# Kernel optimization log

Hardware: AMD Instinct MI355X
Metric: run time of the kernel (lower is better)

## Reference

```python
import jax, jax.numpy as jnp
import numpy as np

D = 256; NH = 8; NL = 4; NP = 4; DFF = 1024; BS = 8; NQ = 300
DH = D // NH
EPS = 1e-5
SPATIAL = np.array([[100, 150], [50, 75], [25, 38], [13, 19]], dtype=np.int64)  # (H, W) per level
SIZES = (SPATIAL[:, 0] * SPATIAL[:, 1])
S = int(SIZES.sum())  # 19947
LSI = np.concatenate([[0], np.cumsum(SIZES)[:-1]]).astype(np.int64)


def setup_inputs() -> dict:
    key = jax.random.key(0)
    ks = iter(jax.random.split(key, 48))
    def nrm(shape, s=0.02):
        return jax.random.normal(next(ks), shape, jnp.float32) * s
    return {
        "tgt": jax.random.normal(next(ks), (BS, NQ, D), jnp.float32),
        "tgt_query_pos": jax.random.normal(next(ks), (BS, NQ, D), jnp.float32),
        "tgt_reference_points": jax.random.uniform(next(ks), (BS, NQ, NL, 2), jnp.float32),
        "memory": jax.random.normal(next(ks), (BS, S, D), jnp.float32),
        "memory_key_padding_mask": jnp.zeros((BS, S), jnp.bool_),
        "memory_spatial_shapes": jnp.asarray(SPATIAL),
        "memory_level_start_index": jnp.asarray(LSI),
        # self-attention (nn.MultiheadAttention) params
        "in_proj_w": nrm((3 * D, D)), "in_proj_b": jnp.zeros((3 * D,), jnp.float32),
        "out_proj_w": nrm((D, D)), "out_proj_b": jnp.zeros((D,), jnp.float32),
        # layernorms
        "norm1_g": jnp.ones((D,), jnp.float32), "norm1_b": jnp.zeros((D,), jnp.float32),
        "norm2_g": jnp.ones((D,), jnp.float32), "norm2_b": jnp.zeros((D,), jnp.float32),
        "norm3_g": jnp.ones((D,), jnp.float32), "norm3_b": jnp.zeros((D,), jnp.float32),
        # MSDeformAttn params
        "samp_off_w": nrm((NH * NL * NP * 2, D)), "samp_off_b": nrm((NH * NL * NP * 2,), 0.5),
        "attn_wt_w": nrm((NH * NL * NP, D)), "attn_wt_b": jnp.zeros((NH * NL * NP,), jnp.float32),
        "value_w": nrm((D, D)), "value_b": jnp.zeros((D,), jnp.float32),
        "outp_w": nrm((D, D)), "outp_b": jnp.zeros((D,), jnp.float32),
        # FFN params
        "lin1_w": nrm((DFF, D)), "lin1_b": jnp.zeros((DFF,), jnp.float32),
        "lin2_w": nrm((D, DFF)), "lin2_b": jnp.zeros((D,), jnp.float32),
    }


def _ln(x, g, b):
    m = x.mean(-1, keepdims=True)
    v = ((x - m) ** 2).mean(-1, keepdims=True)
    return (x - m) / jnp.sqrt(v + EPS) * g + b


def _self_attn(tgt, pos, in_w, in_b, ow, ob):
    bs, nq, _ = tgt.shape
    qk = tgt + pos
    qw, kw, vw = jnp.split(in_w, 3, axis=0)
    qb, kb, vb = jnp.split(in_b, 3)
    proj = lambda x, w, b: (x @ w.T + b).reshape(bs, nq, NH, DH)
    qh, kh, vh = proj(qk, qw, qb), proj(qk, kw, kb), proj(tgt, vw, vb)
    logits = jnp.einsum('bqhd,bkhd->bhqk', qh, kh) / np.sqrt(DH).astype(np.float32)
    a = jax.nn.softmax(logits, axis=-1)
    o = jnp.einsum('bhqk,bkhd->bqhd', a, vh).reshape(bs, nq, D)
    return o @ ow.T + ob


def _msdeform(query, ref, memory, pad_mask, so_w, so_b, aw_w, aw_b, vw, vb, ow, ob):
    bs, nq, _ = query.shape
    value = memory @ vw.T + vb
    value = jnp.where(pad_mask[..., None], 0.0, value).reshape(bs, S, NH, DH)
    off = (query @ so_w.T + so_b).reshape(bs, nq, NH, NL, NP, 2)
    aw = jax.nn.softmax((query @ aw_w.T + aw_b).reshape(bs, nq, NH, NL * NP), axis=-1)
    aw = aw.reshape(bs, nq, NH, NL, NP)
    # offset normalizer is (W, H) per level
    normalizer = jnp.asarray(SPATIAL[:, ::-1].copy(), jnp.float32)
    locs = ref[:, :, None, :, None, :] + off / normalizer[None, None, None, :, None, :]
    out = jnp.zeros((bs, nq, NH, DH), jnp.float32)
    for l in range(NL):
        Hl, Wl = int(SPATIAL[l, 0]), int(SPATIAL[l, 1])
        s0 = int(LSI[l])
        v = value[:, s0:s0 + Hl * Wl]  # [bs, Hl*Wl, NH, DH]
        # grid_sample(align_corners=False) pixel mapping
        x = locs[:, :, :, l, :, 0] * Wl - 0.5  # [bs, nq, NH, NP]
        y = locs[:, :, :, l, :, 1] * Hl - 0.5
        x0f, y0f = jnp.floor(x), jnp.floor(y)
        tx, ty = x - x0f, y - y0f
        x0, y0 = x0f.astype(jnp.int32), y0f.astype(jnp.int32)
        samp = jnp.zeros(x.shape + (DH,), jnp.float32)
        for dy, dx, w in ((0, 0, (1 - ty) * (1 - tx)), (0, 1, (1 - ty) * tx),
                          (1, 0, ty * (1 - tx)), (1, 1, ty * tx)):
            xi, yi = x0 + dx, y0 + dy
            valid = (xi >= 0) & (xi < Wl) & (yi >= 0) & (yi < Hl)  # zero padding
            idx = jnp.clip(yi, 0, Hl - 1) * Wl + jnp.clip(xi, 0, Wl - 1)
            idx2 = idx.swapaxes(2, 3).reshape(bs, nq * NP, NH)
            g = jnp.take_along_axis(v, idx2[..., None], axis=1)  # [bs, nq*NP, NH, DH]
            g = g.reshape(bs, nq, NP, NH, DH).transpose(0, 1, 3, 2, 4)
            samp = samp + g * (w * valid)[..., None]
        out = out + jnp.einsum('bqhp,bqhpd->bqhd', aw[:, :, :, l], samp)
    return out.reshape(bs, nq, D) @ ow.T + ob


def reference(tgt, tgt_query_pos, tgt_reference_points, memory, memory_key_padding_mask,
              memory_spatial_shapes, memory_level_start_index,
              in_proj_w, in_proj_b, out_proj_w, out_proj_b,
              norm1_g, norm1_b, norm2_g, norm2_b, norm3_g, norm3_b,
              samp_off_w, samp_off_b, attn_wt_w, attn_wt_b,
              value_w, value_b, outp_w, outp_b,
              lin1_w, lin1_b, lin2_w, lin2_b):
    # self-cross ordering (self_cross=True), eval mode (dropout=identity)
    t2 = _self_attn(tgt, tgt_query_pos, in_proj_w, in_proj_b, out_proj_w, out_proj_b)
    tgt = _ln(tgt + t2, norm2_g, norm2_b)
    t2 = _msdeform(tgt + tgt_query_pos, tgt_reference_points, memory, memory_key_padding_mask,
                   samp_off_w, samp_off_b, attn_wt_w, attn_wt_b, value_w, value_b, outp_w, outp_b)
    tgt = _ln(tgt + t2, norm1_g, norm1_b)
    t2 = jax.nn.relu(tgt @ lin1_w.T + lin1_b) @ lin2_w.T + lin2_b
    return _ln(tgt + t2, norm3_g, norm3_b)
```

## Files before the change

### kernel.cpp

```cpp
#include <hip/hip_runtime.h>
#include <hip/hip_bf16.h>

#define D_   256
#define NH_  8
#define NL_  4
#define NP_  4
#define DFF_ 1024
#define BS_  8
#define NQ_  300
#define DH_  32
#define S_TOT 19947
#define EPS_ 1e-5f

typedef __bf16 bf16x8 __attribute__((ext_vector_type(8)));
typedef __bf16 bf16x4 __attribute__((ext_vector_type(4)));
typedef float  f32x4  __attribute__((ext_vector_type(4)));

#define W_INW  0
#define W_OUTW 196608
#define W_SOW  262144
#define W_AWW  327680
#define W_VW   360448
#define W_OPW  425984
#define W_L1W  491520
#define W_L2W  753664
#define W_TOT  1015808

__global__ __launch_bounds__(256) void cast_w_kernel(
    const float* __restrict__ s_inw, const float* __restrict__ s_outw,
    const float* __restrict__ s_sow, const float* __restrict__ s_aww,
    const float* __restrict__ s_vw,  const float* __restrict__ s_opw,
    const float* __restrict__ s_l1w, const float* __restrict__ s_l2w,
    __bf16* __restrict__ dst)
{
    const int i = (blockIdx.x * 256 + threadIdx.x) * 4;
    if (i >= W_TOT) return;
    const float* s; int off;
    if      (i < W_OUTW) { s = s_inw;  off = W_INW;  }
    else if (i < W_SOW)  { s = s_outw; off = W_OUTW; }
    else if (i < W_AWW)  { s = s_sow;  off = W_SOW;  }
    else if (i < W_VW)   { s = s_aww;  off = W_AWW;  }
    else if (i < W_OPW)  { s = s_vw;   off = W_VW;   }
    else if (i < W_L1W)  { s = s_opw;  off = W_OPW;  }
    else if (i < W_L2W)  { s = s_l1w;  off = W_L1W;  }
    else                 { s = s_l2w;  off = W_L2W;  }
    const float4 v = *(const float4*)(s + (i - off));
    bf16x4 o;
    o[0] = (__bf16)v.x; o[1] = (__bf16)v.y;
    o[2] = (__bf16)v.z; o[3] = (__bf16)v.w;
    *(bf16x4*)(dst + i) = o;
}

__global__ __launch_bounds__(256) void rearrange_vw_kernel(
    const __bf16* __restrict__ W, __bf16* __restrict__ Wf)
{
    const int g = blockIdx.x * 256 + threadIdx.x;
    const int l = g & 63;
    const int t = (g >> 6) & 15;
    const int s = g >> 10;
    const int row = t * 16 + (l & 15);
    const int col = s * 32 + (l >> 4) * 8;
    *(bf16x8*)(Wf + (size_t)g * 8) = *(const bf16x8*)(W + (size_t)row * 256 + col);
}

__global__ __launch_bounds__(512, 4) void gemm_value(
    const float* __restrict__ A, const __bf16* __restrict__ Wf,
    const float* __restrict__ bias, __hip_bfloat16* __restrict__ C, int M)
{
    __shared__ __align__(16) __bf16 As[2][16][264];
    const int tid = threadIdx.x;
    const int wave = tid >> 6, lane = tid & 63;
    const int frow = lane & 15;
    const int k8 = (lane >> 4) * 8;

    bf16x8 bB[2][8];
#pragma unroll
    for (int j = 0; j < 2; ++j) {
        const int t = wave * 2 + j;
#pragma unroll
        for (int s = 0; s < 8; ++s)
            bB[j][s] = *(const bf16x8*)(Wf + ((size_t)(s * 16 + t) * 64 + lane) * 8);
    }
    float bb0 = bias[wave * 32 + frow];
    float bb1 = bias[wave * 32 + 16 + frow];

    const int nt = (M + 15) >> 4;
    const int stride = gridDim.x;
    int tile = blockIdx.x;

    const int srow = tid >> 5;
    const int scol = (tid & 31) * 8;

    {
        int gr = tile * 16 + srow; if (gr >= M) gr = M - 1;
        const float* ap = A + (size_t)gr * 256 + scol;
        const float4 a0 = *(const float4*)ap;
        const float4 a1 = *(const float4*)(ap + 4);
        bf16x8 o;
        o[0] = (__bf16)a0.x; o[1] = (__bf16)a0.y;
        o[2] = (__bf16)a0.z; o[3] = (__bf16)a0.w;
        o[4] = (__bf16)a1.x; o[5] = (__bf16)a1.y;
        o[6] = (__bf16)a1.z; o[7] = (__bf16)a1.w;
        *(bf16x8*)&As[0][srow][scol] = o;
    }
    __syncthreads();

    int buf = 0;
    for (; tile < nt; tile += stride, buf ^= 1) {
        const int nxt = tile + stride;
        const bool have_nxt = nxt < nt;
        float4 p0, p1;
        if (have_nxt) {
            int gr = nxt * 16 + srow; if (gr >= M) gr = M - 1;
            const float* ap = A + (size_t)gr * 256 + scol;
            p0 = *(const float4*)ap;
            p1 = *(const float4*)(ap + 4);
        }

        f32x4 acc0 = (f32x4){0.f, 0.f, 0.f, 0.f};
        f32x4 acc1 = acc0;
#pragma unroll
        for (int s = 0; s < 8; ++s) {
            const bf16x8 aF = *(const bf16x8*)&As[buf][frow][s * 32 + k8];
            acc0 = __builtin_amdgcn_mfma_f32_16x16x32_bf16(aF, bB[0][s], acc0, 0, 0, 0);
            acc1 = __builtin_amdgcn_mfma_f32_16x16x32_bf16(aF, bB[1][s], acc1, 0, 0, 0);
        }

        const int m0 = tile * 16;
        const int row0 = (lane >> 4) * 4;
        const int col0 = wave * 32 + frow;
#pragma unroll
        for (int r = 0; r < 4; ++r) {
            const int gr = m0 + row0 + r;
            if (gr < M) {
                __hip_bfloat16* cp = C + (size_t)gr * 256 + col0;
                cp[0]  = __float2bfloat16(acc0[r] + bb0);
                cp[16] = __float2bfloat16(acc1[r] + bb1);
            }
        }

        if (have_nxt) {
            bf16x8 o;
            o[0] = (__bf16)p0.x; o[1] = (__bf16)p0.y;
            o[2] = (__bf16)p0.z; o[3] = (__bf16)p0.w;
            o[4] = (__bf16)p1.x; o[5] = (__bf16)p1.y;
            o[6] = (__bf16)p1.z; o[7] = (__bf16)p1.w;
            *(bf16x8*)&As[buf ^ 1][srow][scol] = o;
        }
        __syncthreads();
    }
}

__global__ __launch_bounds__(256) void gemm_small(
    const float* __restrict__ A, const float* __restrict__ A2,
    const __bf16* __restrict__ W, const float* __restrict__ bias,
    float* __restrict__ C, int M, int N, int K, int relu,
    const float* __restrict__ bias2, float* __restrict__ C2, int N1)
{
    __shared__ __align__(16) __bf16 As[64][40];
    __shared__ __align__(16) __bf16 Bs[64][40];
    const int tid = threadIdx.x;
    const int wave = tid >> 6, lane = tid & 63;
    const int m0 = blockIdx.x * 64, n0 = blockIdx.y * 64;
    const int frow = lane & 15, fk = (lane >> 4) * 8;

    f32x4 acc[4];
#pragma unroll
    for (int j = 0; j < 4; ++j) acc[j] = (f32x4){0.f, 0.f, 0.f, 0.f};

    const int ar = tid >> 2;
    const int ak = (tid & 3) * 8;
    const bool a_ok = (m0 + ar) < M;

    for (int k0 = 0; k0 < K; k0 += 32) {
        float4 a0 = make_float4(0,0,0,0), a1 = a0;
        if (a_ok) {
            const float* ap = A + (size_t)(m0 + ar) * K + k0 + ak;
            a0 = *(const float4*)ap;
            a1 = *(const float4*)(ap + 4);
            if (A2) {
                const float* ap2 = A2 + (size_t)(m0 + ar) * K + k0 + ak;
                const float4 c0 = *(const float4*)ap2;
                const float4 c1 = *(const float4*)(ap2 + 4);
                a0.x += c0.x; a0.y += c0.y; a0.z += c0.z; a0.w += c0.w;
                a1.x += c1.x; a1.y += c1.y; a1.z += c1.z; a1.w += c1.w;
            }
        }
        const bf16x8 b8 = *(const bf16x8*)(W + (size_t)(n0 + ar) * K + k0 + ak);

        __syncthreads();
        bf16x8 w0;
        w0[0] = (__bf16)a0.x; w0[1] = (__bf16)a0.y; w0[2] = (__bf16)a0.z; w0[3] = (__bf16)a0.w;
        w0[4] = (__bf16)a1.x; w0[5] = (__bf16)a1.y; w0[6] = (__bf16)a1.z; w0[7] = (__bf16)a1.w;
        *(bf16x8*)&As[ar][ak] = w0;
        *(bf16x8*)&Bs[ar][ak] = b8;
        __syncthreads();

        const bf16x8 aF = *(const bf16x8*)&As[wave * 16 + frow][fk];
#pragma unroll
        for (int j = 0; j < 4; ++j) {
            const bf16x8 bF = *(const bf16x8*)&Bs[j * 16 + frow][fk];
            acc[j] = __builtin_amdgcn_mfma_f32_16x16x32_bf16(aF, bF, acc[j], 0, 0, 0);
        }
    }

    const int row = m0 + wave * 16 + (lane >> 4) * 4;
#pragma unroll
    for (int j = 0; j < 4; ++j) {
        const int col = n0 + j * 16 + frow;
        float* dst; const float* bsrc; int strideC, ccol;
        if (!C2 || col < N1) { dst = C;  bsrc = bias;  strideC = N1;     ccol = col; }
        else                 { dst = C2; bsrc = bias2; strideC = N - N1; ccol = col - N1; }
        const float bb = bsrc[ccol];
#pragma unroll
        for (int r = 0; r < 4; ++r) {
            if (row + r >= M) continue;
            float val = acc[j][r] + bb;
            if (relu) val = fmaxf(val, 0.f);
            dst[(size_t)(row + r) * strideC + ccol] = val;
        }
    }
}

__global__ __launch_bounds__(256) void attn_fused_kernel(
    const float* __restrict__ qk, const float* __restrict__ v,
    float* __restrict__ attn)
{
    __shared__ __align__(16) __bf16 Vt[32][328];
    __shared__ __align__(16) __bf16 Ps[64][328];
    const int qt = blockIdx.x, bh = blockIdx.y;
    const int b = bh >> 3, h = bh & 7;
    const int tid = threadIdx.x;
    const int wave = tid >> 6, lane = tid & 63;
    const float scale = 0.17677669529663687f;

    {
        const int d = tid & 31;
        for (int kk = tid >> 5; kk < NQ_; kk += 8)
            Vt[d][kk] = (__bf16)v[(size_t)(b * NQ_ + kk) * 256 + h * 32 + d];
        for (int i = tid; i < 32 * 20; i += 256)
            Vt[i & 31][300 + (i >> 5)] = (__bf16)0.f;
        for (int i = tid; i < 64 * 16; i += 256)
            Ps[i & 63][304 + (i >> 6)] = (__bf16)0.f;
    }

    const int m = qt * 64 + wave * 16 + (lane & 15);
    const int k8 = (lane >> 4) * 8;

    bf16x8 aF = {};
    if (m < NQ_) {
        const float* qp = qk + (size_t)(b * NQ_ + m) * 512 + h * 32 + k8;
        const float4 q0 = *(const float4*)qp;
        const float4 q1 = *(const float4*)(qp + 4);
        aF[0] = (__bf16)q0.x; aF[1] = (__bf16)q0.y;
        aF[2] = (__bf16)q0.z; aF[3] = (__bf16)q0.w;
        aF[4] = (__bf16)q1.x; aF[5] = (__bf16)q1.y;
        aF[6] = (__bf16)q1.z; aF[7] = (__bf16)q1.w;
    }

    f32x4 c[19];
#pragma unroll
    for (int t = 0; t < 19; ++t) {
        const int n = t * 16 + (lane & 15);
        bf16x8 bF = {};
        if (n < NQ_) {
            const float* kp = qk + (size_t)(b * NQ_ + n) * 512 + 256 + h * 32 + k8;
            const float4 k0 = *(const float4*)kp;
            const float4 k1 = *(const float4*)(kp + 4);
            bF[0] = (__bf16)k0.x; bF[1] = (__bf16)k0.y;
            bF[2] = (__bf16)k0.z; bF[3] = (__bf16)k0.w;
            bF[4] = (__bf16)k1.x; bF[5] = (__bf16)k1.y;
            bF[6] = (__bf16)k1.z; bF[7] = (__bf16)k1.w;
        }
        f32x4 z = (f32x4){0.f, 0.f, 0.f, 0.f};
        c[t] = __builtin_amdgcn_mfma_f32_16x16x32_bf16(aF, bF, z, 0, 0, 0);
    }

    const int myc = lane & 15;
#pragma unroll
    for (int t = 0; t < 19; ++t) {
        const bool ok = (t * 16 + myc) < NQ_;
#pragma unroll
        for (int r = 0; r < 4; ++r)
            c[t][r] = ok ? c[t][r] * scale : -1e30f;
    }

    float mx[4] = {-1e30f, -1e30f, -1e30f, -1e30f};
#pragma unroll
    for (int t = 0; t < 19; ++t)
#pragma unroll
        for (int r = 0; r < 4; ++r) mx[r] = fmaxf(mx[r], c[t][r]);
#pragma unroll
    for (int off = 8; off; off >>= 1)
#pragma unroll
        for (int r = 0; r < 4; ++r)
            mx[r] = fmaxf(mx[r], __shfl_xor(mx[r], off, 64));

    float sum[4] = {0.f, 0.f, 0.f, 0.f};
#pragma unroll
    for (int t = 0; t < 19; ++t)
#pragma unroll
        for (int r = 0; r < 4; ++r) {
            const float e = __expf(c[t][r] - mx[r]);
            c[t][r] = e;
            sum[r] += e;
        }
#pragma unroll
    for (int off = 8; off; off >>= 1)
#pragma unroll
        for (int r = 0; r < 4; ++r)
            sum[r] += __shfl_xor(sum[r], off, 64);
    float inv[4];
#pragma unroll
    for (int r = 0; r < 4; ++r) inv[r] = 1.f / sum[r];

    const int lrow0 = wave * 16 + (lane >> 4) * 4;
#pragma unroll
    for (int t = 0; t < 19; ++t) {
        const int col = t * 16 + myc;
#pragma unroll
        for (int r = 0; r < 4; ++r)
            Ps[lrow0 + r][col] = (__bf16)(c[t][r] * inv[r]);
    }
    __syncthreads();

    const int lm = wave * 16 + (lane & 15);
    f32x4 acc0 = (f32x4){0.f, 0.f, 0.f, 0.f};
    f32x4 acc1 = acc0;
#pragma unroll
    for (int k0 = 0; k0 < 320; k0 += 32) {
        const bf16x8 pF = *(const bf16x8*)&Ps[lm][k0 + k8];
        const bf16x8 b0 = *(const bf16x8*)&Vt[lane & 15][k0 + k8];
        const bf16x8 b1 = *(const bf16x8*)&Vt[16 + (lane & 15)][k0 + k8];
        acc0 = __builtin_amdgcn_mfma_f32_16x16x32_bf16(pF, b0, acc0, 0, 0, 0);
        acc1 = __builtin_amdgcn_mfma_f32_16x16x32_bf16(pF, b1, acc1, 0, 0, 0);
    }

    const int row0 = qt * 64 + lrow0;
    const int col = lane & 15;
#pragma unroll
    for (int r = 0; r < 4; ++r) {
        if (row0 + r >= NQ_) continue;
        float* op = attn + (size_t)(b * NQ_ + row0 + r) * 256 + h * 32;
        op[col]      = acc0[r];
        op[col + 16] = acc1[r];
    }
}

__global__ __launch_bounds__(256) void ln_kernel(
    const float* __restrict__ x, const float* __restrict__ res,
    const float* __restrict__ g, const float* __restrict__ bt,
    float* __restrict__ out,
    const float* __restrict__ pos, float* __restrict__ out2)
{
    const int row = blockIdx.x;
    const int tid = threadIdx.x;
    const size_t idx = (size_t)row * D_ + tid;
    float v = x[idx] + (res ? res[idx] : 0.f);

    __shared__ float red[4];
    float s = v;
#pragma unroll
    for (int off = 32; off; off >>= 1) s += __shfl_xor(s, off, 64);
    if ((tid & 63) == 0) red[tid >> 6] = s;
    __syncthreads();
    const float mean = (red[0] + red[1] + red[2] + red[3]) * (1.f / D_);
    const float c = v - mean;
    __syncthreads();

    float s2 = c * c;
#pragma unroll
    for (int off = 32; off; off >>= 1) s2 += __shfl_xor(s2, off, 64);
    if ((tid & 63) == 0) red[tid >> 6] = s2;
    __syncthreads();
    const float var = (red[0] + red[1] + red[2] + red[3]) * (1.f / D_);

    const float y = c * rsqrtf(var + EPS_) * g[tid] + bt[tid];
    out[idx] = y;
    if (out2) out2[idx] = y + pos[idx];
}

__global__ __launch_bounds__(256) void msdeform_kernel(
    const float* __restrict__ offs, const float* __restrict__ awl,
    const float* __restrict__ refp, const __hip_bfloat16* __restrict__ value,
    float* __restrict__ samp)
{
    const int half = threadIdx.x >> 7;
    const int row = blockIdx.x * 2 + half;
    const int b = row / NQ_;
    const int t = threadIdx.x & 127;
    const int h = t >> 4, d2 = t & 15;

    __shared__ float off_s[2][256];
    __shared__ float aw_s[2][128];
    __shared__ float ref_s[2][8];
    off_s[half][t]       = offs[(size_t)row * 256 + t];
    off_s[half][t + 128] = offs[(size_t)row * 256 + t + 128];
    aw_s[half][t]        = awl[(size_t)row * 128 + t];
    if (t < 8) ref_s[half][t] = refp[(size_t)row * 8 + t];
    __syncthreads();

    float mx = -1e30f;
#pragma unroll
    for (int i = 0; i < 16; ++i) mx = fmaxf(mx, aw_s[half][h * 16 + i]);
    float sum = 0.f;
#pragma unroll
    for (int i = 0; i < 16; ++i) sum += __expf(aw_s[half][h * 16 + i] - mx);
    const float winv = 1.f / sum;

    const int Hs[4] = {100, 50, 25, 13};
    const int Wl_[4] = {150, 75, 38, 19};
    const int S0[4] = {0, 15000, 18750, 19700};

    float o0 = 0.f, o1 = 0.f;
    const __hip_bfloat16* vbase = value + ((size_t)b * S_TOT) * D_ + h * 32 + d2 * 2;

#pragma unroll
    for (int l = 0; l < NL_; ++l) {
        const int Hl = Hs[l], Wl = Wl_[l];
        const float rx = ref_s[half][l * 2], ry = ref_s[half][l * 2 + 1];
        const __hip_bfloat16* vl = vbase + (size_t)S0[l] * D_;
#pragma unroll
        for (int p = 0; p < NP_; ++p) {
            const int oi = ((h * NL_ + l) * NP_ + p) * 2;
            const float lx = rx + off_s[half][oi] / (float)Wl;
            const float ly = ry + off_s[half][oi + 1] / (float)Hl;
            const float x = lx * Wl - 0.5f;
            const float y = ly * Hl - 0.5f;
            const float x0f = floorf(x), y0f = floorf(y);
            const float tx = x - x0f, ty = y - y0f;
            const int x0 = (int)x0f, y0 = (int)y0f;
            const float aw = __expf(aw_s[half][h * 16 + l * 4 + p] - mx) * winv;

            float s0 = 0.f, s1 = 0.f;
#pragma unroll
            for (int cc = 0; cc < 4; ++cc) {
                const int dy = cc >> 1, dx = cc & 1;
                const int xi = x0 + dx, yi = y0 + dy;
                const float w = (dy ? ty : 1.f - ty) * (dx ? tx : 1.f - tx);
                if (xi >= 0 && xi < Wl && yi >= 0 && yi < Hl) {
                    const int idx = yi * Wl + xi;
                    const unsigned u = *(const unsigned*)(vl + (size_t)idx * D_);
                    s0 += w * __uint_as_float(u << 16);
                    s1 += w * __uint_as_float(u & 0xffff0000u);
                }
            }
            o0 += aw * s0;
            o1 += aw * s1;
        }
    }
    float2 ov; ov.x = o0; ov.y = o1;
    *(float2*)(samp + (size_t)row * 256 + h * 32 + d2 * 2) = ov;
}

extern "C" void kernel_launch(void* const* d_in, const int* in_sizes, int n_in,
                              void* d_out, int out_size, void* d_ws, size_t ws_size,
                              hipStream_t stream)
{
    const float* tgt   = (const float*)d_in[0];
    const float* pos   = (const float*)d_in[1];
    const float* refp  = (const float*)d_in[2];
    const float* memory= (const float*)d_in[3];
    const float* in_w  = (const float*)d_in[7];
    const float* in_b  = (const float*)d_in[8];
    const float* outw  = (const float*)d_in[9];
    const float* outb  = (const float*)d_in[10];
    const float* n1g = (const float*)d_in[11]; const float* n1b = (const float*)d_in[12];
    const float* n2g = (const float*)d_in[13]; const float* n2b = (const float*)d_in[14];
    const float* n3g = (const float*)d_in[15]; const float* n3b = (const float*)d_in[16];
    const float* sow = (const float*)d_in[17]; const float* sob = (const float*)d_in[18];
    const float* aww = (const float*)d_in[19]; const float* awb = (const float*)d_in[20];
    const float* vw  = (const float*)d_in[21]; const float* vb_ = (const float*)d_in[22];
    const float* opw = (const float*)d_in[23]; const float* opb = (const float*)d_in[24];
    const float* l1w = (const float*)d_in[25]; const float* l1b = (const float*)d_in[26];
    const float* l2w = (const float*)d_in[27]; const float* l2b = (const float*)d_in[28];
    float* out = (float*)d_out;

    char* ws = (char*)d_ws;
    size_t o = 0;
    auto alloc = [&](size_t bytes) -> char* {
        char* p = ws + o;
        o += (bytes + 255) & ~(size_t)255;
        return p;
    };

    const int M = BS_ * NQ_;
    __bf16* Wb = (__bf16*)alloc((size_t)W_TOT * 2);
    __bf16* Wf = (__bf16*)alloc((size_t)65536 * 2);
    __hip_bfloat16* value = (__hip_bfloat16*)alloc((size_t)BS_ * S_TOT * D_ * 2);
    float* qk    = (float*)alloc((size_t)M * 512 * 4);
    float* v     = (float*)alloc((size_t)M * 256 * 4);
    float* attn  = (float*)alloc((size_t)M * 256 * 4);
    float* attno = (float*)alloc((size_t)M * 256 * 4);
    float* tgt1  = (float*)alloc((size_t)M * 256 * 4);
    float* query2= (float*)alloc((size_t)M * 256 * 4);
    float* offs  = (float*)alloc((size_t)M * 256 * 4);
    float* awl   = (float*)alloc((size_t)M * 128 * 4);
    float* samp  = (float*)alloc((size_t)M * 256 * 4);
    float* t2m   = (float*)alloc((size_t)M * 256 * 4);
    float* tgt2  = (float*)alloc((size_t)M * 256 * 4);
    float* ffn1  = (float*)alloc((size_t)M * 1024 * 4);
    float* ffn2  = (float*)alloc((size_t)M * 256 * 4);

    const dim3 blk(256);
    const int MB = (M + 63) / 64;

    cast_w_kernel<<<(W_TOT / 4 + 255) / 256, blk, 0, stream>>>(
        in_w, outw, sow, aww, vw, opw, l1w, l2w, Wb);
    rearrange_vw_kernel<<<32, blk, 0, stream>>>(Wb + W_VW, Wf);

    gemm_small<<<dim3(MB, 8), blk, 0, stream>>>(tgt, pos, Wb + W_INW, in_b, qk, M, 512, 256, 0, nullptr, nullptr, 512);
    gemm_small<<<dim3(MB, 4), blk, 0, stream>>>(tgt, nullptr, Wb + W_INW + 512 * 256, in_b + 512, v, M, 256, 256, 0, nullptr, nullptr, 256);
    attn_fused_kernel<<<dim3(5, 64), blk, 0, stream>>>(qk, v, attn);
    gemm_small<<<dim3(MB, 4), blk, 0, stream>>>(attn, nullptr, Wb + W_OUTW, outb, attno, M, 256, 256, 0, nullptr, nullptr, 256);
    ln_kernel<<<M, blk, 0, stream>>>(tgt, attno, n2g, n2b, tgt1, pos, query2);

    gemm_small<<<dim3(MB, 6), blk, 0, stream>>>(query2, nullptr, Wb + W_SOW, sob, offs, M, 384, 256, 0, awb, awl, 256);
    gemm_value<<<dim3(512), dim3(512), 0, stream>>>(memory, Wf, vb_, value, BS_ * S_TOT);
    msdeform_kernel<<<M / 2, blk, 0, stream>>>(offs, awl, refp, value, samp);
    gemm_small<<<dim3(MB, 4), blk, 0, stream>>>(samp, nullptr, Wb + W_OPW, opb, t2m, M, 256, 256, 0, nullptr, nullptr, 256);
    ln_kernel<<<M, blk, 0, stream>>>(tgt1, t2m, n1g, n1b, tgt2, nullptr, nullptr);

    gemm_small<<<dim3(MB, 16), blk, 0, stream>>>(tgt2, nullptr, Wb + W_L1W, l1b, ffn1, M, 1024, 256, 1, nullptr, nullptr, 1024);
    gemm_small<<<dim3(MB, 4), blk, 0, stream>>>(ffn1, nullptr, Wb + W_L2W, l2b, ffn2, M, 256, 1024, 0, nullptr, nullptr, 256);
    ln_kernel<<<M, blk, 0, stream>>>(tgt2, ffn2, n3g, n3b, out, nullptr, nullptr);
}
```

Baseline: 447.6 us.

## Fuse output GEMMs with layernorm, merge QKV GEMMs, fold weight rearrange into cast

Adds a gemm_ln kernel in which each 64-row block computes all 256 output columns, then applies bias, residual add and layernorm in registers. It replaces three gemm_small plus ln_kernel pairs, removing intermediate buffers and kernel launches. The QK and V projections become a single launch that uses A2 only for the N<512 column blocks. The value-weight rearrange is folded into the cast kernel, and gemm_value now prefetches input two tiles ahead instead of one. The trade-off is lower parallelism in gemm_ln, which runs only 38 blocks each holding a 256-column accumulator.

Result: slower. 481.5 us (+7.6%).

```diff
diff --git a/kernel.cpp b/kernel.cpp
--- a/kernel.cpp
+++ b/kernel.cpp
@@ -31,8 +31,26 @@
     const float* __restrict__ s_sow, const float* __restrict__ s_aww,
     const float* __restrict__ s_vw,  const float* __restrict__ s_opw,
     const float* __restrict__ s_l1w, const float* __restrict__ s_l2w,
-    __bf16* __restrict__ dst)
+    __bf16* __restrict__ dst, __bf16* __restrict__ Wf)
 {
+    if (blockIdx.x >= 992) {
+        const int g = (blockIdx.x - 992) * 256 + threadIdx.x;
+        const int l = g & 63;
+        const int t = (g >> 6) & 15;
+        const int s = g >> 10;
+        const int row = t * 16 + (l & 15);
+        const int col = s * 32 + (l >> 4) * 8;
+        const float* src = s_vw + (size_t)row * 256 + col;
+        const float4 v0 = *(const float4*)src;
+        const float4 v1 = *(const float4*)(src + 4);
+        bf16x8 o;
+        o[0] = (__bf16)v0.x; o[1] = (__bf16)v0.y;
+        o[2] = (__bf16)v0.z; o[3] = (__bf16)v0.w;
+        o[4] = (__bf16)v1.x; o[5] = (__bf16)v1.y;
+        o[6] = (__bf16)v1.z; o[7] = (__bf16)v1.w;
+        *(bf16x8*)(Wf + (size_t)g * 8) = o;
+        return;
+    }
     const int i = (blockIdx.x * 256 + threadIdx.x) * 4;
     if (i >= W_TOT) return;
     const float* s; int off;
@@ -51,18 +69,6 @@
     *(bf16x4*)(dst + i) = o;
 }
 
-__global__ __launch_bounds__(256) void rearrange_vw_kernel(
-    const __bf16* __restrict__ W, __bf16* __restrict__ Wf)
-{
-    const int g = blockIdx.x * 256 + threadIdx.x;
-    const int l = g & 63;
-    const int t = (g >> 6) & 15;
-    const int s = g >> 10;
-    const int row = t * 16 + (l & 15);
-    const int col = s * 32 + (l >> 4) * 8;
-    *(bf16x8*)(Wf + (size_t)g * 8) = *(const bf16x8*)(W + (size_t)row * 256 + col);
-}
-
 __global__ __launch_bounds__(512, 4) void gemm_value(
     const float* __restrict__ A, const __bf16* __restrict__ Wf,
     const float* __restrict__ bias, __hip_bfloat16* __restrict__ C, int M)
@@ -81,18 +87,18 @@
         for (int s = 0; s < 8; ++s)
             bB[j][s] = *(const bf16x8*)(Wf + ((size_t)(s * 16 + t) * 64 + lane) * 8);
     }
-    float bb0 = bias[wave * 32 + frow];
-    float bb1 = bias[wave * 32 + 16 + frow];
+    const float bb0 = bias[wave * 32 + frow];
+    const float bb1 = bias[wave * 32 + 16 + frow];
 
     const int nt = (M + 15) >> 4;
     const int stride = gridDim.x;
-    int tile = blockIdx.x;
+    const int t0 = blockIdx.x;
 
     const int srow = tid >> 5;
     const int scol = (tid & 31) * 8;
 
     {
-        int gr = tile * 16 + srow; if (gr >= M) gr = M - 1;
+        int gr = t0 * 16 + srow; if (gr >= M) gr = M - 1;
         const float* ap = A + (size_t)gr * 256 + scol;
         const float4 a0 = *(const float4*)ap;
         const float4 a1 = *(const float4*)(ap + 4);
@@ -103,18 +109,25 @@
         o[6] = (__bf16)a1.z; o[7] = (__bf16)a1.w;
         *(bf16x8*)&As[0][srow][scol] = o;
     }
+    float4 q0 = make_float4(0,0,0,0), q1 = q0;
+    bool haveQ = (t0 + stride) < nt;
+    if (haveQ) {
+        int gr = (t0 + stride) * 16 + srow; if (gr >= M) gr = M - 1;
+        const float* ap = A + (size_t)gr * 256 + scol;
+        q0 = *(const float4*)ap;
+        q1 = *(const float4*)(ap + 4);
+    }
     __syncthreads();
 
     int buf = 0;
-    for (; tile < nt; tile += stride, buf ^= 1) {
-        const int nxt = tile + stride;
-        const bool have_nxt = nxt < nt;
-        float4 p0, p1;
-        if (have_nxt) {
-            int gr = nxt * 16 + srow; if (gr >= M) gr = M - 1;
+    for (int tile = t0; tile < nt; tile += stride, buf ^= 1) {
+        float4 r0 = make_float4(0,0,0,0), r1 = r0;
+        const bool haveR = (tile + 2 * stride) < nt;
+        if (haveR) {
+            int gr = (tile + 2 * stride) * 16 + srow; if (gr >= M) gr = M - 1;
             const float* ap = A + (size_t)gr * 256 + scol;
-            p0 = *(const float4*)ap;
-            p1 = *(const float4*)(ap + 4);
+            r0 = *(const float4*)ap;
+            r1 = *(const float4*)(ap + 4);
         }
 
         f32x4 acc0 = (f32x4){0.f, 0.f, 0.f, 0.f};
@@ -139,15 +152,16 @@
             }
         }
 
-        if (have_nxt) {
+        if (haveQ) {
             bf16x8 o;
-            o[0] = (__bf16)p0.x; o[1] = (__bf16)p0.y;
-            o[2] = (__bf16)p0.z; o[3] = (__bf16)p0.w;
-            o[4] = (__bf16)p1.x; o[5] = (__bf16)p1.y;
-            o[6] = (__bf16)p1.z; o[7] = (__bf16)p1.w;
+            o[0] = (__bf16)q0.x; o[1] = (__bf16)q0.y;
+            o[2] = (__bf16)q0.z; o[3] = (__bf16)q0.w;
+            o[4] = (__bf16)q1.x; o[5] = (__bf16)q1.y;
+            o[6] = (__bf16)q1.z; o[7] = (__bf16)q1.w;
             *(bf16x8*)&As[buf ^ 1][srow][scol] = o;
         }
         __syncthreads();
+        q0 = r0; q1 = r1; haveQ = haveR;
     }
 }
 
@@ -171,6 +185,7 @@
     const int ar = tid >> 2;
     const int ak = (tid & 3) * 8;
     const bool a_ok = (m0 + ar) < M;
+    const bool use_a2 = (A2 != nullptr) && (n0 < N1);
 
     for (int k0 = 0; k0 < K; k0 += 32) {
         float4 a0 = make_float4(0,0,0,0), a1 = a0;
@@ -178,7 +193,7 @@
             const float* ap = A + (size_t)(m0 + ar) * K + k0 + ak;
             a0 = *(const float4*)ap;
             a1 = *(const float4*)(ap + 4);
-            if (A2) {
+            if (use_a2) {
                 const float* ap2 = A2 + (size_t)(m0 + ar) * K + k0 + ak;
                 const float4 c0 = *(const float4*)ap2;
                 const float4 c1 = *(const float4*)(ap2 + 4);
@@ -218,6 +233,122 @@
             float val = acc[j][r] + bb;
             if (relu) val = fmaxf(val, 0.f);
             dst[(size_t)(row + r) * strideC + ccol] = val;
+        }
+    }
+}
+
+__global__ __launch_bounds__(256) void gemm_ln(
+    const float* __restrict__ A, const __bf16* __restrict__ W,
+    const float* __restrict__ bias, const float* __restrict__ res,
+    const float* __restrict__ g, const float* __restrict__ bt,
+    float* __restrict__ out, const float* __restrict__ pos,
+    float* __restrict__ out2, int M, int K)
+{
+    __shared__ __align__(16) __bf16 As[64][40];
+    __shared__ __align__(16) __bf16 Bs[256][40];
+    __shared__ float g_s[256], bt_s[256], bias_s[256];
+    const int tid = threadIdx.x;
+    const int wave = tid >> 6, lane = tid & 63;
+    const int m0 = blockIdx.x * 64;
+    const int frow = lane & 15, fk = (lane >> 4) * 8;
+
+    g_s[tid] = g[tid]; bt_s[tid] = bt[tid]; bias_s[tid] = bias[tid];
+
+    f32x4 acc[16];
+#pragma unroll
+    for (int j = 0; j < 16; ++j) acc[j] = (f32x4){0.f, 0.f, 0.f, 0.f};
+
+    const int ar = tid >> 2;
+    const int ak = (tid & 3) * 8;
+    const bool a_ok = (m0 + ar) < M;
+
+    for (int k0 = 0; k0 < K; k0 += 32) {
+        float4 a0 = make_float4(0,0,0,0), a1 = a0;
+        if (a_ok) {
+            const float* ap = A + (size_t)(m0 + ar) * K + k0 + ak;
+            a0 = *(const float4*)ap;
+            a1 = *(const float4*)(ap + 4);
+        }
+        const __bf16* wp = W + (size_t)tid * K + k0;
+        const bf16x8 b0 = *(const bf16x8*)(wp);
+        const bf16x8 b1 = *(const bf16x8*)(wp + 8);
+        const bf16x8 b2 = *(const bf16x8*)(wp + 16);
+        const bf16x8 b3 = *(const bf16x8*)(wp + 24);
+
+        __syncthreads();
+        bf16x8 w0;
+        w0[0] = (__bf16)a0.x; w0[1] = (__bf16)a0.y; w0[2] = (__bf16)a0.z; w0[3] = (__bf16)a0.w;
+        w0[4] = (__bf16)a1.x; w0[5] = (__bf16)a1.y; w0[6] = (__bf16)a1.z; w0[7] = (__bf16)a1.w;
+        *(bf16x8*)&As[ar][ak] = w0;
+        *(bf16x8*)&Bs[tid][0]  = b0;
+        *(bf16x8*)&Bs[tid][8]  = b1;
+        *(bf16x8*)&Bs[tid][16] = b2;
+        *(bf16x8*)&Bs[tid][24] = b3;
+        __syncthreads();
+
+        const bf16x8 aF = *(const bf16x8*)&As[wave * 16 + frow][fk];
+#pragma unroll
+        for (int j = 0; j < 16; ++j) {
+            const bf16x8 bF = *(const bf16x8*)&Bs[j * 16 + frow][fk];
+            acc[j] = __builtin_amdgcn_mfma_f32_16x16x32_bf16(aF, bF, acc[j], 0, 0, 0);
+        }
+    }
+
+    const int rbase = m0 + wave * 16 + (lane >> 4) * 4;
+#pragma unroll
+    for (int j = 0; j < 16; ++j) {
+        const int col = j * 16 + frow;
+        const float bb = bias_s[col];
+#pragma unroll
+        for (int r = 0; r < 4; ++r) {
+            const int row = rbase + r;
+            const float rv = (row < M) ? res[(size_t)row * 256 + col] : 0.f;
+            acc[j][r] += bb + rv;
+        }
+    }
+
+    float s[4] = {0.f, 0.f, 0.f, 0.f};
+#pragma unroll
+    for (int j = 0; j < 16; ++j)
+#pragma unroll
+        for (int r = 0; r < 4; ++r) s[r] += acc[j][r];
+#pragma unroll
+    for (int off = 8; off; off >>= 1)
+#pragma unroll
+        for (int r = 0; r < 4; ++r) s[r] += __shfl_xor(s[r], off, 64);
+    float mean[4];
+#pragma unroll
+    for (int r = 0; r < 4; ++r) mean[r] = s[r] * (1.f / 256.f);
+
+    float s2[4] = {0.f, 0.f, 0.f, 0.f};
+#pragma unroll
+    for (int j = 0; j < 16; ++j)
+#pragma unroll
+        for (int r = 0; r < 4; ++r) {
+            const float c = acc[j][r] - mean[r];
+            acc[j][r] = c;
+            s2[r] += c * c;
+        }
+#pragma unroll
+    for (int off = 8; off; off >>= 1)
+#pragma unroll
+        for (int r = 0; r < 4; ++r) s2[r] += __shfl_xor(s2[r], off, 64);
+    float rstd[4];
+#pragma unroll
+    for (int r = 0; r < 4; ++r) rstd[r] = rsqrtf(s2[r] * (1.f / 256.f) + EPS_);
+
+#pragma unroll
+    for (int j = 0; j < 16; ++j) {
+        const int col = j * 16 + frow;
+        const float gg = g_s[col], bb = bt_s[col];
+#pragma unroll
+        for (int r = 0; r < 4; ++r) {
+            const int row = rbase + r;
+            if (row >= M) continue;
+            const float y = acc[j][r] * rstd[r] * gg + bb;
+            out[(size_t)row * 256 + col] = y;
+            if (out2)
+                out2[(size_t)row * 256 + col] = y + pos[(size_t)row * 256 + col];
         }
     }
 }
@@ -345,39 +476,6 @@
         op[col]      = acc0[r];
         op[col + 16] = acc1[r];
     }
-}
-
-__global__ __launch_bounds__(256) void ln_kernel(
-    const float* __restrict__ x, const float* __restrict__ res,
-    const float* __restrict__ g, const float* __restrict__ bt,
-    float* __restrict__ out,
-    const float* __restrict__ pos, float* __restrict__ out2)
-{
-    const int row = blockIdx.x;
-    const int tid = threadIdx.x;
-    const size_t idx = (size_t)row * D_ + tid;
-    float v = x[idx] + (res ? res[idx] : 0.f);
-
-    __shared__ float red[4];
-    float s = v;
-#pragma unroll
-    for (int off = 32; off; off >>= 1) s += __shfl_xor(s, off, 64);
-    if ((tid & 63) == 0) red[tid >> 6] = s;
-    __syncthreads();
-    const float mean = (red[0] + red[1] + red[2] + red[3]) * (1.f / D_);
-    const float c = v - mean;
-    __syncthreads();
-
-    float s2 = c * c;
-#pragma unroll
-    for (int off = 32; off; off >>= 1) s2 += __shfl_xor(s2, off, 64);
-    if ((tid & 63) == 0) red[tid >> 6] = s2;
-    __syncthreads();
-    const float var = (red[0] + red[1] + red[2] + red[3]) * (1.f / D_);
-
-    const float y = c * rsqrtf(var + EPS_) * g[tid] + bt[tid];
-    out[idx] = y;
-    if (out2) out2[idx] = y + pos[idx];
 }
 
 __global__ __launch_bounds__(256) void msdeform_kernel(
@@ -491,37 +589,41 @@
     float* qk    = (float*)alloc((size_t)M * 512 * 4);
     float* v     = (float*)alloc((size_t)M * 256 * 4);
     float* attn  = (float*)alloc((size_t)M * 256 * 4);
-    float* attno = (float*)alloc((size_t)M * 256 * 4);
     float* tgt1  = (float*)alloc((size_t)M * 256 * 4);
     float* query2= (float*)alloc((size_t)M * 256 * 4);
     float* offs  = (float*)alloc((size_t)M * 256 * 4);
     float* awl   = (float*)alloc((size_t)M * 128 * 4);
     float* samp  = (float*)alloc((size_t)M * 256 * 4);
-    float* t2m   = (float*)alloc((size_t)M * 256 * 4);
     float* tgt2  = (float*)alloc((size_t)M * 256 * 4);
     float* ffn1  = (float*)alloc((size_t)M * 1024 * 4);
-    float* ffn2  = (float*)alloc((size_t)M * 256 * 4);
 
     const dim3 blk(256);
     const int MB = (M + 63) / 64;
 
-    cast_w_kernel<<<(W_TOT / 4 + 255) / 256, blk, 0, stream>>>(
-        in_w, outw, sow, aww, vw, opw, l1w, l2w, Wb);
-    rearrange_vw_kernel<<<32, blk, 0, stream>>>(Wb + W_VW, Wf);
-
-    gemm_small<<<dim3(MB, 8), blk, 0, stream>>>(tgt, pos, Wb + W_INW, in_b, qk, M, 512, 256, 0, nullptr, nullptr, 512);
-    gemm_small<<<dim3(MB, 4), blk, 0, stream>>>(tgt, nullptr, Wb + W_INW + 512 * 256, in_b + 512, v, M, 256, 256, 0, nullptr, nullptr, 256);
+    cast_w_kernel<<<1024, blk, 0, stream>>>(
+        in_w, outw, sow, aww, vw, opw, l1w, l2w, Wb, Wf);
+
+    gemm_small<<<dim3(MB, 12), blk, 0, stream>>>(
+        tgt, pos, Wb + W_INW, in_b, qk, M, 768, 256, 0, in_b + 512, v, 512);
+
     attn_fused_kernel<<<dim3(5, 64), blk, 0, stream>>>(qk, v, attn);
-    gemm_small<<<dim3(MB, 4), blk, 0, stream>>>(attn, nullptr, Wb + W_OUTW, outb, attno, M, 256, 256, 0, nullptr, nullptr, 256);
-    ln_kernel<<<M, blk, 0, stream>>>(tgt, attno, n2g, n2b, tgt1, pos, query2);
-
-    gemm_small<<<dim3(MB, 6), blk, 0, stream>>>(query2, nullptr, Wb + W_SOW, sob, offs, M, 384, 256, 0, awb, awl, 256);
+
+    gemm_ln<<<MB, blk, 0, stream>>>(
+        attn, Wb + W_OUTW, outb, tgt, n2g, n2b, tgt1, pos, query2, M, 256);
+
+    gemm_small<<<dim3(MB, 6), blk, 0, stream>>>(
+        query2, nullptr, Wb + W_SOW, sob, offs, M, 384, 256, 0, awb, awl, 256);
+
     gemm_value<<<dim3(512), dim3(512), 0, stream>>>(memory, Wf, vb_, value, BS_ * S_TOT);
+
     msdeform_kernel<<<M / 2, blk, 0, stream>>>(offs, awl, refp, value, samp);
-    gemm_small<<<dim3(MB, 4), blk, 0, stream>>>(samp, nullptr, Wb + W_OPW, opb, t2m, M, 256, 256, 0, nullptr, nullptr, 256);
-    ln_kernel<<<M, blk, 0, stream>>>(tgt1, t2m, n1g, n1b, tgt2, nullptr, nullptr);
-
-    gemm_small<<<dim3(MB, 16), blk, 0, stream>>>(tgt2, nullptr, Wb + W_L1W, l1b, ffn1, M, 1024, 256, 1, nullptr, nullptr, 1024);
-    gemm_small<<<dim3(MB, 4), blk, 0, stream>>>(ffn1, nullptr, Wb + W_L2W, l2b, ffn2, M, 256, 1024, 0, nullptr, nullptr, 256);
-    ln_kernel<<<M, blk, 0, stream>>>(tgt2, ffn2, n3g, n3b, out, nullptr, nullptr);
+
+    gemm_ln<<<MB, blk, 0, stream>>>(
+        samp, Wb + W_OPW, opb, tgt1, n1g, n1b, tgt2, nullptr, nullptr, M, 256);
+
+    gemm_small<<<dim3(MB, 16), blk, 0, stream>>>(
+        tgt2, nullptr, Wb + W_L1W, l1b, ffn1, M, 1024, 256, 1, nullptr, nullptr, 1024);
+
+    gemm_ln<<<MB, blk, 0, stream>>>(
+        ffn1, Wb + W_L2W, l2b, tgt2, n3g, n3b, out, nullptr, nullptr, M, 1024);
 }
```
